# Performance work log

Hardware: AMD Instinct MI355X
Metric: run time of the kernel (lower is better)

Reference implementation:

```python
import jax, jax.numpy as jnp
import numpy as np

B = 1024      # graphs (frames)
P = 23        # nodes per frame (22 players + ball)
N = B * P     # total nodes
F = 14        # input node features
D = 256       # hidden dim
H = 4         # attention heads
Dh = D // H   # per-head dim
L = 3         # GATv2 layers
C = 23        # receiver classes
NEG_SLOPE = 0.2


def setup_inputs() -> dict:
    key = jax.random.key(0)
    ks = jax.random.split(key, 20)
    x = jax.random.normal(ks[0], (N, F), jnp.float32)
    # complete directed graph (no self loops) within each frame
    a = np.arange(P)
    s, d = np.meshgrid(a, a, indexing='ij')
    m = s != d
    s, d = s[m], d[m]                      # [P*(P-1)] = 506
    offs = (np.arange(B) * P)[:, None]
    src = (s[None, :] + offs).reshape(-1)
    dst = (d[None, :] + offs).reshape(-1)
    edge_index = jnp.asarray(np.stack([src, dst]), jnp.int32)   # [2, E]
    batch = jnp.asarray(np.repeat(np.arange(B), P), jnp.int32)  # [N]
    g = lambda k, shape, fan: jax.random.normal(k, shape, jnp.float32) / np.sqrt(fan)
    return {
        'x': x, 'edge_index': edge_index, 'batch': batch,
        # input projection F -> D
        'W_in': g(ks[1], (F, D), F), 'b_in': jnp.zeros((D,), jnp.float32),
        # stacked GATv2 layer params (all D -> D)
        'Wl': g(ks[2], (L, D, H, Dh), D), 'Wr': g(ks[3], (L, D, H, Dh), D),
        'att': g(ks[4], (L, H, Dh), Dh),
        # receiver head: D -> D -> C
        'Wr1': g(ks[5], (D, D), D), 'br1': jnp.zeros((D,), jnp.float32),
        'Wr2': g(ks[6], (D, C), D), 'br2': jnp.zeros((C,), jnp.float32),
        # shot head: receiver embedding + concat MLP 2D -> D -> 1
        'E_recv': g(ks[7], (C, D), D),
        'Ws1': g(ks[8], (2 * D, D), 2 * D), 'bs1': jnp.zeros((D,), jnp.float32),
        'Ws2': g(ks[9], (D, 1), D), 'bs2': jnp.zeros((1,), jnp.float32),
    }


def _gatv2_layer(h, src, dst, Wl, Wr, att):
    # GATv2: e_ij = a^T LeakyReLU(Wl h_j + Wr h_i); msg = alpha_ij * Wl h_j
    hl = jnp.einsum('nd,dhk->nhk', h, Wl)               # [N,H,Dh]
    hr = jnp.einsum('nd,dhk->nhk', h, Wr)
    e = jax.nn.leaky_relu(hl[src] + hr[dst], NEG_SLOPE) # [E,H,Dh]
    scores = jnp.einsum('ehk,hk->eh', e, att)           # [E,H]
    # segment softmax over incoming edges of each dst node
    smax = jax.ops.segment_max(scores, dst, num_segments=N)   # [N,H]
    ex = jnp.exp(scores - smax[dst])
    denom = jax.ops.segment_sum(ex, dst, num_segments=N)      # [N,H]
    alpha = ex / denom[dst]                                    # [E,H]
    msg = hl[src] * alpha[..., None]                           # [E,H,Dh]
    out = jax.ops.segment_sum(msg, dst, num_segments=N).reshape(N, H * Dh)
    return jax.nn.elu(out + h)  # residual + activation


def reference(x, edge_index, batch, W_in, b_in, Wl, Wr, att,
              Wr1, br1, Wr2, br2, E_recv, Ws1, bs1, Ws2, bs2):
    src, dst = edge_index[0], edge_index[1]
    h = x @ W_in + b_in                                   # [N,D]
    for l in range(L):
        h = _gatv2_layer(h, src, dst, Wl[l], Wr[l], att[l])
    # mean readout per graph
    cnt = jax.ops.segment_sum(jnp.ones((N,), h.dtype), batch, num_segments=B)
    g = jax.ops.segment_sum(h, batch, num_segments=B) / cnt[:, None]  # [B,D]
    # receiver distribution
    recv_logits = jax.nn.relu(g @ Wr1 + br1) @ Wr2 + br2  # [B,C]
    recv_probs = jax.nn.softmax(recv_logits, axis=1)
    # shot logit for every (graph, receiver) pair, fully batched
    z = jnp.concatenate([
        jnp.broadcast_to(g[:, None, :], (B, C, D)),
        jnp.broadcast_to(E_recv[None, :, :], (B, C, D)),
    ], axis=-1)                                           # [B,C,2D]
    shot_bc = (jax.nn.relu(z @ Ws1 + bs1) @ Ws2 + bs2)[..., 0]  # [B,C]
    # marginalize: expected shot logit under receiver distribution
    return jnp.sum(shot_bc * recv_probs, axis=1)          # [B]
```

## Files before the change

### kernel.cpp

```cpp
#include <hip/hip_runtime.h>

#define BBATCH 1024
#define NPAIR 512
#define PP 23
#define FF 14
#define DD 256
#define CC 23

#define HSTR 258
#define SLSTR 264
#define RG 47472
#define SL_OFF   (RG)
#define SRO_OFF  (RG + 12144)
#define FRAG_OFF (RG)
#define S_OFF    (RG + 24576)
#define XS_OFF   (RG + 24576)
#define SATT_OFF (RG + 33040)
#define SMEM_SZ  (RG + 33568)

#define SWZB(b) ((b) ^ (((b) >> 3) & 7))
#define SWZC(c) (SWZB((c) >> 3) * 8 + ((c) & 7))

typedef _Float16 f16;
typedef __attribute__((ext_vector_type(8))) _Float16 f16x8;
typedef __attribute__((ext_vector_type(4))) _Float16 f16x4;
typedef __attribute__((ext_vector_type(2))) _Float16 f16x2;
typedef __attribute__((ext_vector_type(4))) float f32x4;

__global__ __launch_bounds__(256) void k_prep(const float* __restrict__ Wl,
    const float* __restrict__ Wr, const float* __restrict__ E,
    const float* __restrict__ Ws1, f16* __restrict__ Bf, float* __restrict__ EB)
{
    __shared__ float ws[DD][16];
    int t = threadIdx.x;
    if (blockIdx.x < 96) {
        int bid = blockIdx.x;
        int ll = bid >> 5, ntile = bid & 31;
        int n0 = ntile * 16;
        const float* W = (n0 < 256) ? (Wl + (size_t)ll * 65536) : (Wr + (size_t)ll * 65536);
        int c0 = n0 & 255;
        for (int kk = t >> 4; kk < DD; kk += 16)
            ws[kk][t & 15] = W[(size_t)kk * 256 + c0 + (t & 15)];
        __syncthreads();
        size_t base = (size_t)bid * 4096;
        for (int idx = t; idx < 4096; idx += 256) {
            int ks = idx >> 9;
            int lane = (idx >> 3) & 63;
            int e = idx & 7;
            int col = lane & 15;
            int k = ks * 32 + ((lane >> 4) << 3) + e;
            Bf[base + idx] = (f16)ws[k][col];
        }
    } else {
        int c = blockIdx.x - 96;
        float acc = 0.f;
        for (int k = 0; k < DD; ++k)
            acc = fmaf(E[c * DD + k], Ws1[(DD + k) * DD + t], acc);
        EB[c * DD + t] = acc;
    }
}

__global__ __launch_bounds__(512, 4) void k_fused(
    const float* __restrict__ x, const float* __restrict__ Win,
    const float* __restrict__ bin, const f16* __restrict__ Bf,
    const float* __restrict__ att, float* __restrict__ g)
{
    __shared__ __align__(16) char smem[SMEM_SZ];
    float* hstate = (float*)smem;
    f16* sl16   = (f16*)(smem + SL_OFF);
    f16* sro16  = (f16*)(smem + SRO_OFF);
    f16* frag   = (f16*)(smem + FRAG_OFF);
    float* S    = (float*)(smem + S_OFF);
    float* xs   = (float*)(smem + XS_OFF);
    f16* satt16 = (f16*)(smem + SATT_OFF);

    int t = threadIdx.x;
    int pair = blockIdx.x;

    for (int idx = t; idx < 46 * FF; idx += 512)
        xs[idx] = x[(size_t)pair * 46 * FF + idx];
    __syncthreads();

    {
        int c2 = (t & 127) * 2, rp = t >> 7;
        float2 bb = *(const float2*)&bin[c2];
        for (int r = rp; r < 48; r += 4) {
            float h0 = 0.f, h1 = 0.f;
            if (r < 46) {
                h0 = bb.x; h1 = bb.y;
#pragma unroll
                for (int f = 0; f < FF; ++f) {
                    float xv = xs[r * FF + f];
                    float2 wv = *(const float2*)&Win[f * DD + c2];
                    h0 = fmaf(xv, wv.x, h0);
                    h1 = fmaf(xv, wv.y, h1);
                }
                *(float2*)&hstate[r * HSTR + c2] = make_float2(h0, h1);
            }
            int off = ((r >> 4) * 8 + (c2 >> 5)) * 512 +
                      ((r & 15) + (((c2 & 31) >> 3) << 4)) * 8 + (c2 & 7);
            f16x2 hv2 = { (f16)h0, (f16)h1 };
            *(f16x2*)(frag + off) = hv2;
        }
    }

    int ln = t & 63, w = t >> 6;

    int sc_i  = t >> 4;
    int sc_ch = t & 15;
    int sc_hh = sc_ch >> 2;
    bool sc_act = (t < 368);
    int sb0 = SWZB(2 * sc_ch) * 8;
    int sb1 = SWZB(2 * sc_ch + 1) * 8;

    for (int layer = 0; layer < 3; ++layer) {
        if (t < DD) satt16[SWZC(t)] = (f16)att[layer * DD + t];

        if (layer > 0) {
            int c2 = (t & 127) * 2, rp = t >> 7;
            for (int r = rp; r < 48; r += 4) {
                float h0 = 0.f, h1 = 0.f;
                if (r < 46) {
                    float2 hv = *(const float2*)&hstate[r * HSTR + c2];
                    h0 = hv.x; h1 = hv.y;
                }
                int off = ((r >> 4) * 8 + (c2 >> 5)) * 512 +
                          ((r & 15) + (((c2 & 31) >> 3) << 4)) * 8 + (c2 & 7);
                f16x2 hv2 = { (f16)h0, (f16)h1 };
                *(f16x2*)(frag + off) = hv2;
            }
        }
        __syncthreads();

        const f16* pB = Bf + (size_t)layer * 131072 + (size_t)(w * 4) * 4096 + ln * 8;
        const f16* lA = frag + ln * 8;

        f32x4 acc[3][4];
#pragma unroll
        for (int mt = 0; mt < 3; ++mt)
#pragma unroll
            for (int nt = 0; nt < 4; ++nt) acc[mt][nt] = (f32x4)0.0f;

#pragma unroll
        for (int ks = 0; ks < 8; ++ks) {
            f16x8 a0 = *(const f16x8*)(lA + (0 * 8 + ks) * 512);
            f16x8 a1 = *(const f16x8*)(lA + (1 * 8 + ks) * 512);
            f16x8 a2 = *(const f16x8*)(lA + (2 * 8 + ks) * 512);
#pragma unroll
            for (int nt = 0; nt < 4; ++nt) {
                f16x8 b = *(const f16x8*)(pB + (nt * 8 + ks) * 512);
                acc[0][nt] = __builtin_amdgcn_mfma_f32_16x16x32_f16(a0, b, acc[0][nt], 0, 0, 0);
                acc[1][nt] = __builtin_amdgcn_mfma_f32_16x16x32_f16(a1, b, acc[1][nt], 0, 0, 0);
                acc[2][nt] = __builtin_amdgcn_mfma_f32_16x16x32_f16(a2, b, acc[2][nt], 0, 0, 0);
            }
        }
        __syncthreads();

        for (int f = 0; f < 2; ++f) {
#pragma unroll
            for (int mt = 0; mt < 3; ++mt) {
                int rbase = mt * 16 + (ln >> 4) * 4;
#pragma unroll
                for (int nt = 0; nt < 4; ++nt) {
                    int col = w * 64 + nt * 16 + (ln & 15);
                    f16* dst = (col < 256) ? sl16 : sro16;
                    int cc = col & 255;
                    int sc = SWZC(cc);
#pragma unroll
                    for (int r2 = 0; r2 < 4; ++r2) {
                        int i = rbase + r2 - f * PP;
                        if (0 <= i && i < PP) dst[i * SLSTR + sc] = (f16)acc[mt][nt][r2];
                    }
                }
            }
            __syncthreads();

            if (sc_act) {
                f16x8 av0 = *(const f16x8*)(satt16 + sb0);
                f16x8 av1 = *(const f16x8*)(satt16 + sb1);
                const f16* srp = sro16 + sc_i * SLSTR;
                f16x8 rv0 = *(const f16x8*)(srp + sb0);
                f16x8 rv1 = *(const f16x8*)(srp + sb1);
                for (int j = 0; j < PP; ++j) {
                    const f16* slp = sl16 + j * SLSTR;
                    f16x8 v0 = *(const f16x8*)(slp + sb0) + rv0;
                    f16x8 v1 = *(const f16x8*)(slp + sb1) + rv1;
                    v0 = __builtin_elementwise_max(v0, v0 * (f16)0.2f);
                    v1 = __builtin_elementwise_max(v1, v1 * (f16)0.2f);
                    f16x8 tot = av0 * v0;
                    tot += av1 * v1;
                    f16x4 t4 = __builtin_shufflevector(tot, tot, 0, 1, 2, 3) +
                               __builtin_shufflevector(tot, tot, 4, 5, 6, 7);
                    float p = (float)t4[0] + (float)t4[1] + (float)t4[2] + (float)t4[3];
                    p += __shfl_xor(p, 1, 64);
                    p += __shfl_xor(p, 2, 64);
                    if ((t & 3) == 0)
                        S[(sc_i * PP + j) * 4 + sc_hh] = (j == sc_i) ? -1e30f : p;
                }
            }
            __syncthreads();

            if (t < 368) {
                int i = t >> 4, hh = (t >> 2) & 3, q = t & 3;
                float m = -1e30f;
                for (int j = q; j < PP; j += 4)
                    m = fmaxf(m, S[(i * PP + j) * 4 + hh]);
                m = fmaxf(m, __shfl_xor(m, 1, 64));
                m = fmaxf(m, __shfl_xor(m, 2, 64));
                float s = 0.f;
                for (int j = q; j < PP; j += 4)
                    s += __expf(S[(i * PP + j) * 4 + hh] - m);
                s += __shfl_xor(s, 1, 64);
                s += __shfl_xor(s, 2, 64);
                float inv = 1.f / s;
                for (int j = q; j < PP; j += 4) {
                    float* p = S + (i * PP + j) * 4 + hh;
                    *p = __expf(*p - m) * inv;
                }
            }
            __syncthreads();

            {
                int c = t & 255, ip = t >> 8, hh = c >> 6;
                int scn = SWZC(c);
                float slc[PP];
#pragma unroll
                for (int j = 0; j < PP; ++j) slc[j] = (float)sl16[j * SLSTR + scn];
                for (int i = ip; i < PP; i += 2) {
                    float accv = 0.f;
#pragma unroll
                    for (int j = 0; j < PP; ++j)
                        accv = fmaf(S[(i * PP + j) * 4 + hh], slc[j], accv);
                    int r = f * PP + i;
                    float res = accv + hstate[r * HSTR + c];
                    hstate[r * HSTR + c] = (res > 0.f) ? res : (__expf(res) - 1.f);
                }
            }
            __syncthreads();
        }
    }

    {
        int f = t >> 8, c = t & 255;
        float s = 0.f;
#pragma unroll
        for (int i = 0; i < PP; ++i) s += hstate[(f * PP + i) * HSTR + c];
        g[(size_t)(pair * 2 + f) * DD + c] = s * (1.0f / 23.0f);
    }
}

__global__ __launch_bounds__(256) void k_head(const float* __restrict__ g,
    const float* __restrict__ Wr1, const float* __restrict__ br1,
    const float* __restrict__ Wr2, const float* __restrict__ br2,
    const float* __restrict__ Ws1, const float* __restrict__ bs1,
    const float* __restrict__ Ws2, const float* __restrict__ bs2,
    const float* __restrict__ EB, float* __restrict__ out)
{
    __shared__ float gs[4][DD], t1s[4][DD], gtop[4][DD];
    __shared__ float logits[4][CC], probs[4][CC];
    __shared__ float red[4][4];
    int b0 = blockIdx.x * 4;
    int t = threadIdx.x;
    for (int idx = t; idx < 4 * DD; idx += 256)
        gs[idx >> 8][idx & 255] = g[(size_t)b0 * DD + idx];
    __syncthreads();

    float a1[4] = {0.f, 0.f, 0.f, 0.f}, a2[4] = {0.f, 0.f, 0.f, 0.f};
    for (int k = 0; k < DD; k += 2) {
        float w1a = Wr1[k * DD + t], w1b = Wr1[(k + 1) * DD + t];
        float w2a = Ws1[k * DD + t], w2b = Ws1[(k + 1) * DD + t];
#pragma unroll
        for (int gg = 0; gg < 4; ++gg) {
            float2 gv = *(const float2*)&gs[gg][k];
            a1[gg] = fmaf(gv.x, w1a, a1[gg]);
            a1[gg] = fmaf(gv.y, w1b, a1[gg]);
            a2[gg] = fmaf(gv.x, w2a, a2[gg]);
            a2[gg] = fmaf(gv.y, w2b, a2[gg]);
        }
    }
#pragma unroll
    for (int gg = 0; gg < 4; ++gg) {
        t1s[gg][t] = fmaxf(a1[gg] + br1[t], 0.f);
        gtop[gg][t] = a2[gg] + bs1[t];
    }
    __syncthreads();

    if (t < 4 * CC) {
        int gg = t / CC, c = t - gg * CC;
        float acc = br2[c];
        for (int d = 0; d < DD; ++d) acc = fmaf(t1s[gg][d], Wr2[d * CC + c], acc);
        logits[gg][c] = acc;
    }
    __syncthreads();
    if (t < 4 * CC) {
        int gg = t / CC, c = t - gg * CC;
        float m = -1e30f;
        for (int cc = 0; cc < CC; ++cc) m = fmaxf(m, logits[gg][cc]);
        float s = 0.f;
        for (int cc = 0; cc < CC; ++cc) s += __expf(logits[gg][cc] - m);
        probs[gg][c] = __expf(logits[gg][c] - m) / s;
    }
    __syncthreads();

    float wd = Ws2[t];
    float sacc[4];
#pragma unroll
    for (int gg = 0; gg < 4; ++gg) {
        float gt = gtop[gg][t];
        float acc = 0.f;
#pragma unroll
        for (int c = 0; c < CC; ++c)
            acc = fmaf(probs[gg][c], fmaxf(gt + EB[c * DD + t], 0.f), acc);
        sacc[gg] = acc * wd;
    }
#pragma unroll
    for (int gg = 0; gg < 4; ++gg) {
        float v = sacc[gg];
#pragma unroll
        for (int off = 32; off > 0; off >>= 1) v += __shfl_down(v, off, 64);
        if ((t & 63) == 0) red[t >> 6][gg] = v;
    }
    __syncthreads();
    if (t < 4)
        out[b0 + t] = red[0][t] + red[1][t] + red[2][t] + red[3][t] + bs2[0];
}

extern "C" void kernel_launch(void* const* d_in, const int* in_sizes, int n_in,
                              void* d_out, int out_size, void* d_ws, size_t ws_size,
                              hipStream_t stream)
{
    const float* x     = (const float*)d_in[0];
    const float* Win   = (const float*)d_in[3];
    const float* bin   = (const float*)d_in[4];
    const float* Wl    = (const float*)d_in[5];
    const float* Wr    = (const float*)d_in[6];
    const float* att   = (const float*)d_in[7];
    const float* Wr1   = (const float*)d_in[8];
    const float* br1   = (const float*)d_in[9];
    const float* Wr2   = (const float*)d_in[10];
    const float* br2   = (const float*)d_in[11];
    const float* Erecv = (const float*)d_in[12];
    const float* Ws1   = (const float*)d_in[13];
    const float* bs1   = (const float*)d_in[14];
    const float* Ws2   = (const float*)d_in[15];
    const float* bs2   = (const float*)d_in[16];
    float* out = (float*)d_out;

    f16* Bf   = (f16*)d_ws;
    float* g  = (float*)(Bf + (size_t)3 * 131072);
    float* EB = g + (size_t)BBATCH * DD;

    k_prep<<<dim3(96 + CC), dim3(256), 0, stream>>>(Wl, Wr, Erecv, Ws1, Bf, EB);
    k_fused<<<dim3(NPAIR), dim3(512), 0, stream>>>(x, Win, bin, Bf, att, g);
    k_head<<<dim3(256), dim3(256), 0, stream>>>(g, Wr1, br1, Wr2, br2,
                                                Ws1, bs1, Ws2, bs2, EB, out);
}
```

Baseline: 166.1 us.

## Process one frame per block instead of two to shrink shared memory

The fused GATv2 kernel now handles a single 23-node frame per block, launching 1024 blocks instead of 512. The GEMM drops from 3 to 2 M-tiles and the two-frame inner loop goes away. Shared memory shrinks substantially because hstate halves, attention scores are stored in fp16, and att is read straight from global memory, which should allow more resident blocks per CU. The change also adds an XOR swizzle on the A-fragment layout to reduce LDS bank conflicts. In exchange, each Bf weight fragment is fetched twice as often overall, the 32-row tiles waste 9 padding rows, and the fp16 scores and probabilities lose some precision.

```diff
diff --git a/kernel.cpp b/kernel.cpp
--- a/kernel.cpp
+++ b/kernel.cpp
@@ -1,7 +1,6 @@
 #include <hip/hip_runtime.h>
 
 #define BBATCH 1024
-#define NPAIR 512
 #define PP 23
 #define FF 14
 #define DD 256
@@ -9,14 +8,13 @@
 
 #define HSTR 258
 #define SLSTR 264
-#define RG 47472
-#define SL_OFF   (RG)
-#define SRO_OFF  (RG + 12144)
-#define FRAG_OFF (RG)
-#define S_OFF    (RG + 24576)
-#define XS_OFF   (RG + 24576)
-#define SATT_OFF (RG + 33040)
-#define SMEM_SZ  (RG + 33568)
+#define U_OFF 23736
+#define SL_OFF   (U_OFF)
+#define SRO_OFF  (U_OFF + 12144)
+#define FRAG_OFF (U_OFF)
+#define S_OFF    (U_OFF + 24288)
+#define XS_OFF   (S_OFF)
+#define SMEM_SZ  (S_OFF + 4232)
 
 #define SWZB(b) ((b) ^ (((b) >> 3) & 7))
 #define SWZC(c) (SWZB((c) >> 3) * 8 + ((c) & 7))
@@ -26,6 +24,12 @@
 typedef __attribute__((ext_vector_type(4))) _Float16 f16x4;
 typedef __attribute__((ext_vector_type(2))) _Float16 f16x2;
 typedef __attribute__((ext_vector_type(4))) float f32x4;
+
+__device__ __forceinline__ int frag_off(int r, int c) {
+    int u = (r & 15) + (((c & 31) >> 3) << 4);
+    u ^= (u >> 4);
+    return ((r >> 4) * 8 + (c >> 5)) * 512 + u * 8 + (c & 7);
+}
 
 __global__ __launch_bounds__(256) void k_prep(const float* __restrict__ Wl,
     const float* __restrict__ Wr, const float* __restrict__ E,
@@ -70,41 +74,36 @@
     f16* sl16   = (f16*)(smem + SL_OFF);
     f16* sro16  = (f16*)(smem + SRO_OFF);
     f16* frag   = (f16*)(smem + FRAG_OFF);
-    float* S    = (float*)(smem + S_OFF);
+    f16* S16    = (f16*)(smem + S_OFF);
     float* xs   = (float*)(smem + XS_OFF);
-    f16* satt16 = (f16*)(smem + SATT_OFF);
 
     int t = threadIdx.x;
-    int pair = blockIdx.x;
-
-    for (int idx = t; idx < 46 * FF; idx += 512)
-        xs[idx] = x[(size_t)pair * 46 * FF + idx];
+    int frame = blockIdx.x;
+
+    for (int idx = t; idx < PP * FF; idx += 512)
+        xs[idx] = x[(size_t)frame * PP * FF + idx];
     __syncthreads();
 
     {
         int c2 = (t & 127) * 2, rp = t >> 7;
         float2 bb = *(const float2*)&bin[c2];
-        for (int r = rp; r < 48; r += 4) {
-            float h0 = 0.f, h1 = 0.f;
-            if (r < 46) {
-                h0 = bb.x; h1 = bb.y;
-#pragma unroll
-                for (int f = 0; f < FF; ++f) {
-                    float xv = xs[r * FF + f];
-                    float2 wv = *(const float2*)&Win[f * DD + c2];
-                    h0 = fmaf(xv, wv.x, h0);
-                    h1 = fmaf(xv, wv.y, h1);
-                }
-                *(float2*)&hstate[r * HSTR + c2] = make_float2(h0, h1);
-            }
-            int off = ((r >> 4) * 8 + (c2 >> 5)) * 512 +
-                      ((r & 15) + (((c2 & 31) >> 3) << 4)) * 8 + (c2 & 7);
+        for (int r = rp; r < PP; r += 4) {
+            float h0 = bb.x, h1 = bb.y;
+#pragma unroll
+            for (int f = 0; f < FF; ++f) {
+                float xv = xs[r * FF + f];
+                float2 wv = *(const float2*)&Win[f * DD + c2];
+                h0 = fmaf(xv, wv.x, h0);
+                h1 = fmaf(xv, wv.y, h1);
+            }
+            *(float2*)&hstate[r * HSTR + c2] = make_float2(h0, h1);
             f16x2 hv2 = { (f16)h0, (f16)h1 };
-            *(f16x2*)(frag + off) = hv2;
+            *(f16x2*)(frag + frag_off(r, c2)) = hv2;
         }
     }
 
     int ln = t & 63, w = t >> 6;
+    int lnsw = (ln ^ (ln >> 4)) * 8;
 
     int sc_i  = t >> 4;
     int sc_ch = t & 15;
@@ -114,30 +113,22 @@
     int sb1 = SWZB(2 * sc_ch + 1) * 8;
 
     for (int layer = 0; layer < 3; ++layer) {
-        if (t < DD) satt16[SWZC(t)] = (f16)att[layer * DD + t];
-
         if (layer > 0) {
             int c2 = (t & 127) * 2, rp = t >> 7;
-            for (int r = rp; r < 48; r += 4) {
-                float h0 = 0.f, h1 = 0.f;
-                if (r < 46) {
-                    float2 hv = *(const float2*)&hstate[r * HSTR + c2];
-                    h0 = hv.x; h1 = hv.y;
-                }
-                int off = ((r >> 4) * 8 + (c2 >> 5)) * 512 +
-                          ((r & 15) + (((c2 & 31) >> 3) << 4)) * 8 + (c2 & 7);
-                f16x2 hv2 = { (f16)h0, (f16)h1 };
-                *(f16x2*)(frag + off) = hv2;
+            for (int r = rp; r < PP; r += 4) {
+                float2 hv = *(const float2*)&hstate[r * HSTR + c2];
+                f16x2 hv2 = { (f16)hv.x, (f16)hv.y };
+                *(f16x2*)(frag + frag_off(r, c2)) = hv2;
             }
         }
         __syncthreads();
 
         const f16* pB = Bf + (size_t)layer * 131072 + (size_t)(w * 4) * 4096 + ln * 8;
-        const f16* lA = frag + ln * 8;
-
-        f32x4 acc[3][4];
-#pragma unroll
-        for (int mt = 0; mt < 3; ++mt)
+        const f16* lA = frag + lnsw;
+
+        f32x4 acc[2][4];
+#pragma unroll
+        for (int mt = 0; mt < 2; ++mt)
 #pragma unroll
             for (int nt = 0; nt < 4; ++nt) acc[mt][nt] = (f32x4)0.0f;
 
@@ -145,107 +136,109 @@
         for (int ks = 0; ks < 8; ++ks) {
             f16x8 a0 = *(const f16x8*)(lA + (0 * 8 + ks) * 512);
             f16x8 a1 = *(const f16x8*)(lA + (1 * 8 + ks) * 512);
-            f16x8 a2 = *(const f16x8*)(lA + (2 * 8 + ks) * 512);
 #pragma unroll
             for (int nt = 0; nt < 4; ++nt) {
                 f16x8 b = *(const f16x8*)(pB + (nt * 8 + ks) * 512);
                 acc[0][nt] = __builtin_amdgcn_mfma_f32_16x16x32_f16(a0, b, acc[0][nt], 0, 0, 0);
                 acc[1][nt] = __builtin_amdgcn_mfma_f32_16x16x32_f16(a1, b, acc[1][nt], 0, 0, 0);
-                acc[2][nt] = __builtin_amdgcn_mfma_f32_16x16x32_f16(a2, b, acc[2][nt], 0, 0, 0);
-            }
-        }
-        __syncthreads();
-
-        for (int f = 0; f < 2; ++f) {
-#pragma unroll
-            for (int mt = 0; mt < 3; ++mt) {
-                int rbase = mt * 16 + (ln >> 4) * 4;
-#pragma unroll
-                for (int nt = 0; nt < 4; ++nt) {
-                    int col = w * 64 + nt * 16 + (ln & 15);
-                    f16* dst = (col < 256) ? sl16 : sro16;
-                    int cc = col & 255;
-                    int sc = SWZC(cc);
-#pragma unroll
-                    for (int r2 = 0; r2 < 4; ++r2) {
-                        int i = rbase + r2 - f * PP;
-                        if (0 <= i && i < PP) dst[i * SLSTR + sc] = (f16)acc[mt][nt][r2];
-                    }
+            }
+        }
+        __syncthreads();
+
+#pragma unroll
+        for (int mt = 0; mt < 2; ++mt) {
+            int rbase = mt * 16 + (ln >> 4) * 4;
+#pragma unroll
+            for (int nt = 0; nt < 4; ++nt) {
+                int col = w * 64 + nt * 16 + (ln & 15);
+                f16* dst = (col < 256) ? sl16 : sro16;
+                int cc = col & 255;
+                int sc = SWZC(cc);
+#pragma unroll
+                for (int r2 = 0; r2 < 4; ++r2) {
+                    int i = rbase + r2;
+                    if (i < PP) dst[i * SLSTR + sc] = (f16)acc[mt][nt][r2];
                 }
             }
-            __syncthreads();
-
-            if (sc_act) {
-                f16x8 av0 = *(const f16x8*)(satt16 + sb0);
-                f16x8 av1 = *(const f16x8*)(satt16 + sb1);
-                const f16* srp = sro16 + sc_i * SLSTR;
-                f16x8 rv0 = *(const f16x8*)(srp + sb0);
-                f16x8 rv1 = *(const f16x8*)(srp + sb1);
-                for (int j = 0; j < PP; ++j) {
-                    const f16* slp = sl16 + j * SLSTR;
-                    f16x8 v0 = *(const f16x8*)(slp + sb0) + rv0;
-                    f16x8 v1 = *(const f16x8*)(slp + sb1) + rv1;
-                    v0 = __builtin_elementwise_max(v0, v0 * (f16)0.2f);
-                    v1 = __builtin_elementwise_max(v1, v1 * (f16)0.2f);
-                    f16x8 tot = av0 * v0;
-                    tot += av1 * v1;
-                    f16x4 t4 = __builtin_shufflevector(tot, tot, 0, 1, 2, 3) +
-                               __builtin_shufflevector(tot, tot, 4, 5, 6, 7);
-                    float p = (float)t4[0] + (float)t4[1] + (float)t4[2] + (float)t4[3];
-                    p += __shfl_xor(p, 1, 64);
-                    p += __shfl_xor(p, 2, 64);
-                    if ((t & 3) == 0)
-                        S[(sc_i * PP + j) * 4 + sc_hh] = (j == sc_i) ? -1e30f : p;
-                }
-            }
-            __syncthreads();
-
-            if (t < 368) {
-                int i = t >> 4, hh = (t >> 2) & 3, q = t & 3;
-                float m = -1e30f;
-                for (int j = q; j < PP; j += 4)
-                    m = fmaxf(m, S[(i * PP + j) * 4 + hh]);
-                m = fmaxf(m, __shfl_xor(m, 1, 64));
-                m = fmaxf(m, __shfl_xor(m, 2, 64));
-                float s = 0.f;
-                for (int j = q; j < PP; j += 4)
-                    s += __expf(S[(i * PP + j) * 4 + hh] - m);
-                s += __shfl_xor(s, 1, 64);
-                s += __shfl_xor(s, 2, 64);
-                float inv = 1.f / s;
-                for (int j = q; j < PP; j += 4) {
-                    float* p = S + (i * PP + j) * 4 + hh;
-                    *p = __expf(*p - m) * inv;
-                }
-            }
-            __syncthreads();
-
-            {
-                int c = t & 255, ip = t >> 8, hh = c >> 6;
-                int scn = SWZC(c);
-                float slc[PP];
-#pragma unroll
-                for (int j = 0; j < PP; ++j) slc[j] = (float)sl16[j * SLSTR + scn];
-                for (int i = ip; i < PP; i += 2) {
-                    float accv = 0.f;
-#pragma unroll
-                    for (int j = 0; j < PP; ++j)
-                        accv = fmaf(S[(i * PP + j) * 4 + hh], slc[j], accv);
-                    int r = f * PP + i;
-                    float res = accv + hstate[r * HSTR + c];
-                    hstate[r * HSTR + c] = (res > 0.f) ? res : (__expf(res) - 1.f);
-                }
-            }
-            __syncthreads();
-        }
-    }
-
-    {
-        int f = t >> 8, c = t & 255;
+        }
+        __syncthreads();
+
+        if (sc_act) {
+            const float* ap = att + layer * DD + sc_ch * 16;
+            float4 af0 = *(const float4*)(ap);
+            float4 af1 = *(const float4*)(ap + 4);
+            float4 af2 = *(const float4*)(ap + 8);
+            float4 af3 = *(const float4*)(ap + 12);
+            f16x8 av0 = { (f16)af0.x, (f16)af0.y, (f16)af0.z, (f16)af0.w,
+                          (f16)af1.x, (f16)af1.y, (f16)af1.z, (f16)af1.w };
+            f16x8 av1 = { (f16)af2.x, (f16)af2.y, (f16)af2.z, (f16)af2.w,
+                          (f16)af3.x, (f16)af3.y, (f16)af3.z, (f16)af3.w };
+            const f16* srp = sro16 + sc_i * SLSTR;
+            f16x8 rv0 = *(const f16x8*)(srp + sb0);
+            f16x8 rv1 = *(const f16x8*)(srp + sb1);
+            for (int j = 0; j < PP; ++j) {
+                const f16* slp = sl16 + j * SLSTR;
+                f16x8 v0 = *(const f16x8*)(slp + sb0) + rv0;
+                f16x8 v1 = *(const f16x8*)(slp + sb1) + rv1;
+                v0 = __builtin_elementwise_max(v0, v0 * (f16)0.2f);
+                v1 = __builtin_elementwise_max(v1, v1 * (f16)0.2f);
+                f16x8 tot = av0 * v0;
+                tot += av1 * v1;
+                f16x4 t4 = __builtin_shufflevector(tot, tot, 0, 1, 2, 3) +
+                           __builtin_shufflevector(tot, tot, 4, 5, 6, 7);
+                float p = (float)t4[0] + (float)t4[1] + (float)t4[2] + (float)t4[3];
+                p += __shfl_xor(p, 1, 64);
+                p += __shfl_xor(p, 2, 64);
+                if ((t & 3) == 0)
+                    S16[(sc_i * PP + j) * 4 + sc_hh] =
+                        (j == sc_i) ? (f16)(-60000.0f) : (f16)p;
+            }
+        }
+        __syncthreads();
+
+        if (t < 368) {
+            int i = t >> 4, hh = (t >> 2) & 3, q = t & 3;
+            float m = -1e30f;
+            for (int j = q; j < PP; j += 4)
+                m = fmaxf(m, (float)S16[(i * PP + j) * 4 + hh]);
+            m = fmaxf(m, __shfl_xor(m, 1, 64));
+            m = fmaxf(m, __shfl_xor(m, 2, 64));
+            float s = 0.f;
+            for (int j = q; j < PP; j += 4)
+                s += __expf((float)S16[(i * PP + j) * 4 + hh] - m);
+            s += __shfl_xor(s, 1, 64);
+            s += __shfl_xor(s, 2, 64);
+            float inv = 1.f / s;
+            for (int j = q; j < PP; j += 4) {
+                f16* p = S16 + (i * PP + j) * 4 + hh;
+                *p = (f16)(__expf((float)*p - m) * inv);
+            }
+        }
+        __syncthreads();
+
+        {
+            int c = t & 255, ip = t >> 8, hh = c >> 6;
+            int scn = SWZC(c);
+            float slc[PP];
+#pragma unroll
+            for (int j = 0; j < PP; ++j) slc[j] = (float)sl16[j * SLSTR + scn];
+            for (int i = ip; i < PP; i += 2) {
+                float accv = 0.f;
+#pragma unroll
+                for (int j = 0; j < PP; ++j)
+                    accv = fmaf((float)S16[(i * PP + j) * 4 + hh], slc[j], accv);
+                float res = accv + hstate[i * HSTR + c];
+                hstate[i * HSTR + c] = (res > 0.f) ? res : (__expf(res) - 1.f);
+            }
+        }
+        __syncthreads();
+    }
+
+    if (t < DD) {
         float s = 0.f;
 #pragma unroll
-        for (int i = 0; i < PP; ++i) s += hstate[(f * PP + i) * HSTR + c];
-        g[(size_t)(pair * 2 + f) * DD + c] = s * (1.0f / 23.0f);
+        for (int i = 0; i < PP; ++i) s += hstate[i * HSTR + t];
+        g[(size_t)frame * DD + t] = s * (1.0f / 23.0f);
     }
 }
 
@@ -351,7 +344,7 @@
     float* EB = g + (size_t)BBATCH * DD;
 
     k_prep<<<dim3(96 + CC), dim3(256), 0, stream>>>(Wl, Wr, Erecv, Ws1, Bf, EB);
-    k_fused<<<dim3(NPAIR), dim3(512), 0, stream>>>(x, Win, bin, Bf, att, g);
+    k_fused<<<dim3(BBATCH), dim3(512), 0, stream>>>(x, Win, bin, Bf, att, g);
     k_head<<<dim3(256), dim3(256), 0, stream>>>(g, Wr1, br1, Wr2, br2,
                                                 Ws1, bs1, Ws2, bs2, EB, out);
 }
```

After: 227.5 us. 1.37x slower.

## Compute attention aggregation with MFMA using fp16 alpha in fragment layout

Applied to the files above, without the earlier changes.

The per-node weighted sum of neighbor features, previously scalar fp32 FMAs over an fp32 score buffer, now runs on 16x16x32 f16 MFMA instructions. Scores and softmax weights are stored as fp16 directly in the MFMA A-fragment layout, zero-initialised once so padded neighbor slots contribute nothing. The attention vector is now read from global memory and converted in registers, which removes its shared-memory staging buffer. In exchange the softmax weights lose precision (fp16, with a -60000 diagonal mask), and the B fragments are built from strided scalar shared-memory reads.

```diff
diff --git a/kernel.cpp b/kernel.cpp
--- a/kernel.cpp
+++ b/kernel.cpp
@@ -10,13 +10,12 @@
 #define HSTR 258
 #define SLSTR 264
 #define RG 47472
-#define SL_OFF   (RG)
-#define SRO_OFF  (RG + 12144)
-#define FRAG_OFF (RG)
-#define S_OFF    (RG + 24576)
-#define XS_OFF   (RG + 24576)
-#define SATT_OFF (RG + 33040)
-#define SMEM_SZ  (RG + 33568)
+#define SL_OFF    (RG)
+#define SRO_OFF   (RG + 12144)
+#define FRAG_OFF  (RG)
+#define ALPHA_OFF (RG + 24576)
+#define XS_OFF    (ALPHA_OFF)
+#define SMEM_SZ   (ALPHA_OFF + 8192)
 
 #define SWZB(b) ((b) ^ (((b) >> 3) & 7))
 #define SWZC(c) (SWZB((c) >> 3) * 8 + ((c) & 7))
@@ -70,9 +69,8 @@
     f16* sl16   = (f16*)(smem + SL_OFF);
     f16* sro16  = (f16*)(smem + SRO_OFF);
     f16* frag   = (f16*)(smem + FRAG_OFF);
-    float* S    = (float*)(smem + S_OFF);
+    f16* aF     = (f16*)(smem + ALPHA_OFF);
     float* xs   = (float*)(smem + XS_OFF);
-    f16* satt16 = (f16*)(smem + SATT_OFF);
 
     int t = threadIdx.x;
     int pair = blockIdx.x;
@@ -114,8 +112,6 @@
     int sb1 = SWZB(2 * sc_ch + 1) * 8;
 
     for (int layer = 0; layer < 3; ++layer) {
-        if (t < DD) satt16[SWZC(t)] = (f16)att[layer * DD + t];
-
         if (layer > 0) {
             int c2 = (t & 127) * 2, rp = t >> 7;
             for (int r = rp; r < 48; r += 4) {
@@ -132,6 +128,9 @@
         }
         __syncthreads();
 
+        if (layer == 0)
+            *(f32x4*)(smem + ALPHA_OFF + t * 16) = (f32x4)0.f;
+
         const f16* pB = Bf + (size_t)layer * 131072 + (size_t)(w * 4) * 4096 + ln * 8;
         const f16* lA = frag + ln * 8;
 
@@ -176,11 +175,20 @@
             __syncthreads();
 
             if (sc_act) {
-                f16x8 av0 = *(const f16x8*)(satt16 + sb0);
-                f16x8 av1 = *(const f16x8*)(satt16 + sb1);
+                const float* ap = att + layer * DD + sc_ch * 16;
+                float4 af0 = *(const float4*)(ap);
+                float4 af1 = *(const float4*)(ap + 4);
+                float4 af2 = *(const float4*)(ap + 8);
+                float4 af3 = *(const float4*)(ap + 12);
+                f16x8 av0 = { (f16)af0.x, (f16)af0.y, (f16)af0.z, (f16)af0.w,
+                              (f16)af1.x, (f16)af1.y, (f16)af1.z, (f16)af1.w };
+                f16x8 av1 = { (f16)af2.x, (f16)af2.y, (f16)af2.z, (f16)af2.w,
+                              (f16)af3.x, (f16)af3.y, (f16)af3.z, (f16)af3.w };
                 const f16* srp = sro16 + sc_i * SLSTR;
                 f16x8 rv0 = *(const f16x8*)(srp + sb0);
                 f16x8 rv1 = *(const f16x8*)(srp + sb1);
+                int wbase = ((sc_hh * 2 + (sc_i >> 4)) << 9) + ((sc_i & 15) << 3);
+#pragma unroll 2
                 for (int j = 0; j < PP; ++j) {
                     const f16* slp = sl16 + j * SLSTR;
                     f16x8 v0 = *(const f16x8*)(slp + sb0) + rv0;
@@ -195,45 +203,57 @@
                     p += __shfl_xor(p, 1, 64);
                     p += __shfl_xor(p, 2, 64);
                     if ((t & 3) == 0)
-                        S[(sc_i * PP + j) * 4 + sc_hh] = (j == sc_i) ? -1e30f : p;
+                        aF[wbase + ((j >> 3) << 7) + (j & 7)] =
+                            (j == sc_i) ? (f16)(-60000.0f) : (f16)p;
                 }
             }
             __syncthreads();
 
             if (t < 368) {
                 int i = t >> 4, hh = (t >> 2) & 3, q = t & 3;
+                int base = ((hh * 2 + (i >> 4)) << 9) + ((i & 15) << 3);
                 float m = -1e30f;
                 for (int j = q; j < PP; j += 4)
-                    m = fmaxf(m, S[(i * PP + j) * 4 + hh]);
+                    m = fmaxf(m, (float)aF[base + ((j >> 3) << 7) + (j & 7)]);
                 m = fmaxf(m, __shfl_xor(m, 1, 64));
                 m = fmaxf(m, __shfl_xor(m, 2, 64));
                 float s = 0.f;
                 for (int j = q; j < PP; j += 4)
-                    s += __expf(S[(i * PP + j) * 4 + hh] - m);
+                    s += __expf((float)aF[base + ((j >> 3) << 7) + (j & 7)] - m);
                 s += __shfl_xor(s, 1, 64);
                 s += __shfl_xor(s, 2, 64);
                 float inv = 1.f / s;
                 for (int j = q; j < PP; j += 4) {
-                    float* p = S + (i * PP + j) * 4 + hh;
-                    *p = __expf(*p - m) * inv;
+                    f16* p = aF + base + ((j >> 3) << 7) + (j & 7);
+                    *p = (f16)(__expf((float)*p - m) * inv);
                 }
             }
             __syncthreads();
 
             {
-                int c = t & 255, ip = t >> 8, hh = c >> 6;
-                int scn = SWZC(c);
-                float slc[PP];
-#pragma unroll
-                for (int j = 0; j < PP; ++j) slc[j] = (float)sl16[j * SLSTR + scn];
-                for (int i = ip; i < PP; i += 2) {
-                    float accv = 0.f;
-#pragma unroll
-                    for (int j = 0; j < PP; ++j)
-                        accv = fmaf(S[(i * PP + j) * 4 + hh], slc[j], accv);
-                    int r = f * PP + i;
-                    float res = accv + hstate[r * HSTR + c];
-                    hstate[r * HSTR + c] = (res > 0.f) ? res : (__expf(res) - 1.f);
+                int h = w >> 1, mt = w & 1;
+                f16x8 afrag = *(const f16x8*)(aF + ((h * 2 + mt) << 9) + ln * 8);
+                int k0 = (ln >> 4) * 8;
+                int cb = h * 64 + (ln & 15);
+#pragma unroll
+                for (int nt = 0; nt < 4; ++nt) {
+                    int c = cb + nt * 16;
+                    int scn = SWZC(c);
+                    f16x8 bfrag;
+#pragma unroll
+                    for (int e = 0; e < 8; ++e)
+                        bfrag[e] = sl16[(k0 + e) * SLSTR + scn];
+                    f32x4 a4 = __builtin_amdgcn_mfma_f32_16x16x32_f16(
+                        afrag, bfrag, (f32x4)0.0f, 0, 0, 0);
+#pragma unroll
+                    for (int r2 = 0; r2 < 4; ++r2) {
+                        int i = mt * 16 + (ln >> 4) * 4 + r2;
+                        if (i < PP) {
+                            int r = f * PP + i;
+                            float res = a4[r2] + hstate[r * HSTR + c];
+                            hstate[r * HSTR + c] = (res > 0.f) ? res : (__expf(res) - 1.f);
+                        }
+                    }
                 }
             }
             __syncthreads();
```

Result: faster. 152.4 us (-8.3%).
